# Kernel optimization log

Hardware: AMD Instinct MI355X
Metric: run time of the kernel (lower is better)

## Reference

```python
import jax, jax.numpy as jnp
import numpy as np

# ---- module constants (from init_kwargs) ----
L = 16            # num_levels
T = 524288        # table_size (power of 2 -> uint32 wraparound-safe mod)
DIN = 3
FPL = 2           # FEATURES_PER_LEVEL
GRID_MIN, GRID_MAX = -1.0, 1.0
B = 262144

RES = jnp.asarray(np.exp(np.linspace(np.log(16.0), np.log(2048.0), L)), dtype=jnp.float32)  # (L,)
PRIMES = jnp.array([1, 2654435761, 805459861], dtype=jnp.uint32)                            # (3,)
# offsets match torch: format(i, '03b') -> MSB first
OFFSETS = jnp.array([[(i >> (DIN - 1 - d)) & 1 for d in range(DIN)] for i in range(2 ** DIN)], dtype=jnp.uint32)  # (8,3)
OFF_F = OFFSETS.astype(jnp.float32)
OFF_HASH = (OFFSETS * PRIMES).sum(-1)  # (8,) uint32; hash is linear in coords so corner offsets separate out


def setup_inputs() -> dict:
    key = jax.random.key(0)
    ks = jax.random.split(key, 8)
    return {
        "x": jax.random.uniform(ks[0], (B, DIN), jnp.float32, minval=GRID_MIN, maxval=GRID_MAX),
        "embeddings": jax.random.uniform(ks[1], (L, T, FPL), jnp.float32, minval=-1e-4, maxval=1e-4),
        "W1": jax.random.normal(ks[2], (64, L * FPL), jnp.float32) * (1.0 / np.sqrt(L * FPL)),
        "b1": jax.random.normal(ks[3], (64,), jnp.float32) * 0.01,
        "W2": jax.random.normal(ks[4], (64, 64), jnp.float32) * (1.0 / 8.0),
        "b2": jax.random.normal(ks[5], (64,), jnp.float32) * 0.01,
        "Wout": jax.random.normal(ks[6], (1, 64), jnp.float32) * (1.0 / 8.0),
        "bout": jax.random.normal(ks[7], (1,), jnp.float32) * 0.01,
    }


def reference(x, embeddings, W1, b1, W2, b2, Wout, bout):
    n = x.shape[0]
    x_norm = (x - GRID_MIN) / (GRID_MAX - GRID_MIN)          # (B,3) in [0,1)
    x_grid = x_norm[None, :, :] * RES[:, None, None]          # (L,B,3)
    x0 = jnp.floor(x_grid)
    w = x_grid - x0                                           # (L,B,3) fractional part
    # hashed = ((x0+offset) . primes) % T ; linear -> split base + offset hash (uint32 wrap == low bits of int64)
    base = (x0.astype(jnp.uint32) * PRIMES).sum(-1)           # (L,B)
    hashed = ((base[:, :, None] + OFF_HASH) % T).astype(jnp.int32)   # (L,B,8)
    corners = jnp.take_along_axis(
        embeddings, hashed.reshape(L, -1, 1), axis=1
    ).reshape(L, n, 2 ** DIN, FPL)                            # (L,B,8,2)
    # trilinear weights: prod over dims of (1-off) + w*(2*off-1)
    per_dim = 1.0 - OFF_F + w[:, :, None, :] * (2.0 * OFF_F - 1.0)   # (L,B,8,3)
    cw = per_dim.prod(-1)                                     # (L,B,8)
    value = jnp.einsum('lbc,lbcf->lbf', cw, corners)          # (L,B,2)
    encoded = jnp.moveaxis(value, 0, 1).reshape(n, L * FPL)   # (B,32)
    h = jax.nn.silu(encoded @ W1.T + b1)
    h = jax.nn.silu(h @ W2.T + b2)
    return (h @ Wout.T + bout).squeeze(-1)                    # (B,)
```

## Files before the change

kernel.cpp:

```cpp
#include <hip/hip_runtime.h>
#include <math.h>
#include <stdint.h>

#define NLEV 16
#define TBL 524288
#define TMASK (TBL - 1)
#define BLOCK 256
#define SPT 4
#define P1 2654435761u
#define P2 805459861u

struct ResArr { float r[NLEV]; };

typedef __attribute__((ext_vector_type(4))) float f32x4;
typedef __attribute__((ext_vector_type(8))) short bf16x8;
struct __attribute__((packed, aligned(8))) f4wrap { f32x4 v; };

__device__ __forceinline__ float silu_f(float v) {
    return __fdividef(v, 1.0f + __expf(-v));
}

__device__ __forceinline__ uint32_t f2bf(float f) {
    uint32_t u = __float_as_uint(f);
    return (u + 0x7FFFu + ((u >> 16) & 1u)) >> 16;
}
__device__ __forceinline__ float bf2f(uint32_t b) {
    return __uint_as_float(b << 16);
}
__device__ __forceinline__ void split_bf(float x, bf16x8& hi, bf16x8& lo, int e) {
    const uint32_t hb = f2bf(x);
    hi[e] = (short)hb;
    lo[e] = (short)f2bf(x - bf2f(hb));
}

__global__ void __launch_bounds__(BLOCK)
encode_kernel(const float* __restrict__ x,
              const float* __restrict__ emb,
              uint32_t* __restrict__ enc_ws,
              int nsamp, ResArr res)
{
    const int bid = blockIdx.x;
    const int xcd = bid & 7;
    const int j   = bid >> 3;
    int lvl, chunk;
    if (j < 352) {
        const int F = xcd * 352 + j;
        lvl = 5 + (F >> 8);
        chunk = F & 255;
    } else {
        const int C = xcd * 160 + (j - 352);
        lvl = C >> 8;
        chunk = C & 255;
    }

    const int t  = threadIdx.x;
    const int s0 = chunk * (BLOCK * SPT) + t;
    const float rs = res.r[lvl];
    const float* tabf = emb + (size_t)lvl * TBL * 2;

    uint32_t i0[SPT][4];
    float w0[SPT], w1[SPT], w2[SPT];
    uint32_t bad = 0;

    #pragma unroll
    for (int p = 0; p < SPT; ++p) {
        const int s = s0 + p * BLOCK;
        const float xv0 = __builtin_nontemporal_load(&x[(size_t)s * 3 + 0]);
        const float xv1 = __builtin_nontemporal_load(&x[(size_t)s * 3 + 1]);
        const float xv2 = __builtin_nontemporal_load(&x[(size_t)s * 3 + 2]);
        const float g0 = (xv0 + 1.0f) * 0.5f * rs;
        const float g1 = (xv1 + 1.0f) * 0.5f * rs;
        const float g2 = (xv2 + 1.0f) * 0.5f * rs;
        const float f0 = floorf(g0), f1 = floorf(g1), f2 = floorf(g2);
        w0[p] = g0 - f0; w1[p] = g1 - f1; w2[p] = g2 - f2;
        const uint32_t hb = (uint32_t)f0 + (uint32_t)f1 * P1 + (uint32_t)f2 * P2;
        #pragma unroll
        for (int q = 0; q < 4; ++q) {
            uint32_t h = hb;
            if ((q >> 1) & 1) h += P1;
            if (q & 1)        h += P2;
            i0[p][q] = h & TMASK;
            bad |= (uint32_t)(i0[p][q] == TMASK);
        }
    }

    f32x4 v[SPT][4];
    if (__builtin_expect(__any((int)bad), 0)) {
        #pragma unroll
        for (int p = 0; p < SPT; ++p)
            #pragma unroll
            for (int q = 0; q < 4; ++q) {
                const uint32_t a = i0[p][q];
                const uint32_t b = (a + 1u) & TMASK;
                const float2 lo = *(const float2*)(tabf + 2 * (size_t)a);
                const float2 hi = *(const float2*)(tabf + 2 * (size_t)b);
                v[p][q] = f32x4{lo.x, lo.y, hi.x, hi.y};
            }
    } else {
        #pragma unroll
        for (int p = 0; p < SPT; ++p)
            #pragma unroll
            for (int q = 0; q < 4; ++q)
                v[p][q] = ((const f4wrap*)(tabf + 2 * (size_t)i0[p][q]))->v;
    }

    #pragma unroll
    for (int p = 0; p < SPT; ++p) {
        const float om0 = 1.0f - w0[p], om1 = 1.0f - w1[p], om2 = 1.0f - w2[p];
        float e0 = 0.0f, e1 = 0.0f;
        #pragma unroll
        for (int q = 0; q < 4; ++q) {
            float wb = (((q >> 1) & 1) ? w1[p] : om1) * ((q & 1) ? w2[p] : om2);
            const float c0 = om0 * wb;
            const float c1 = w0[p] * wb;
            e0 = fmaf(c0, v[p][q].x, fmaf(c1, v[p][q].z, e0));
            e1 = fmaf(c0, v[p][q].y, fmaf(c1, v[p][q].w, e1));
        }
        const int s = s0 + p * BLOCK;
        const uint32_t pk = f2bf(e0) | (f2bf(e1) << 16);
        __builtin_nontemporal_store(pk, &enc_ws[(size_t)lvl * nsamp + s]);
    }
}

__global__ void __launch_bounds__(BLOCK)
mlp_mfma_kernel(const uint32_t* __restrict__ enc_ws,
                const float* __restrict__ W1,
                const float* __restrict__ b1,
                const float* __restrict__ W2,
                const float* __restrict__ b2,
                const float* __restrict__ Wout,
                const float* __restrict__ bout,
                float* __restrict__ out, int nsamp)
{
    __shared__ __align__(16) unsigned short hbuf[4][32 * 72];

    const int tid  = threadIdx.x;
    const int wid  = tid >> 6;
    const int lane = tid & 63;
    const int l15  = lane & 15;
    const int g    = lane >> 4;
    const int sbase = blockIdx.x * 128 + wid * 32;
    unsigned short* hw = hbuf[wid];

    bf16x8 b1hi[4], b1lo[4];
    float  b1v[4];
    #pragma unroll
    for (int n = 0; n < 4; ++n) {
        const float* wr = W1 + (n * 16 + l15) * 32 + g * 8;
        const f32x4 wv0 = ((const f4wrap*)wr)->v;
        const f32x4 wv1 = ((const f4wrap*)(wr + 4))->v;
        #pragma unroll
        for (int e = 0; e < 4; ++e) {
            split_bf(wv0[e], b1hi[n], b1lo[n], e);
            split_bf(wv1[e], b1hi[n], b1lo[n], e + 4);
        }
        b1v[n] = b1[n * 16 + l15];
    }

    #pragma unroll
    for (int m = 0; m < 2; ++m) {
        union { uint32_t u[4]; bf16x8 v; } af;
        const int s = sbase + m * 16 + l15;
        #pragma unroll
        for (int d = 0; d < 4; ++d)
            af.u[d] = enc_ws[(size_t)(g * 4 + d) * nsamp + s];
        #pragma unroll
        for (int n = 0; n < 4; ++n) {
            f32x4 acc = {0.f, 0.f, 0.f, 0.f};
            acc = __builtin_amdgcn_mfma_f32_16x16x32_bf16(af.v, b1lo[n], acc, 0, 0, 0);
            acc = __builtin_amdgcn_mfma_f32_16x16x32_bf16(af.v, b1hi[n], acc, 0, 0, 0);
            #pragma unroll
            for (int r = 0; r < 4; ++r) {
                const int row = m * 16 + g * 4 + r;
                const int col = n * 16 + l15;
                hw[row * 72 + col] = (unsigned short)f2bf(silu_f(acc[r] + b1v[n]));
            }
        }
    }

    f32x4 acc2[2][4];
    #pragma unroll
    for (int m = 0; m < 2; ++m)
        #pragma unroll
        for (int n = 0; n < 4; ++n)
            acc2[m][n] = f32x4{0.f, 0.f, 0.f, 0.f};

    #pragma unroll
    for (int ks = 0; ks < 2; ++ks) {
        bf16x8 b2hi[4], b2lo[4];
        #pragma unroll
        for (int n = 0; n < 4; ++n) {
            const float* wr = W2 + (n * 16 + l15) * 64 + ks * 32 + g * 8;
            const f32x4 wv0 = ((const f4wrap*)wr)->v;
            const f32x4 wv1 = ((const f4wrap*)(wr + 4))->v;
            #pragma unroll
            for (int e = 0; e < 4; ++e) {
                split_bf(wv0[e], b2hi[n], b2lo[n], e);
                split_bf(wv1[e], b2hi[n], b2lo[n], e + 4);
            }
        }
        #pragma unroll
        for (int m = 0; m < 2; ++m) {
            const bf16x8 a2 = *(const bf16x8*)&hw[(m * 16 + l15) * 72 + ks * 32 + g * 8];
            #pragma unroll
            for (int n = 0; n < 4; ++n) {
                acc2[m][n] = __builtin_amdgcn_mfma_f32_16x16x32_bf16(a2, b2lo[n], acc2[m][n], 0, 0, 0);
                acc2[m][n] = __builtin_amdgcn_mfma_f32_16x16x32_bf16(a2, b2hi[n], acc2[m][n], 0, 0, 0);
            }
        }
    }

    float b2v[4], wov[4];
    #pragma unroll
    for (int n = 0; n < 4; ++n) {
        b2v[n] = b2[n * 16 + l15];
        wov[n] = Wout[n * 16 + l15];
    }
    const float bo = bout[0];

    #pragma unroll
    for (int m = 0; m < 2; ++m) {
        float part[4] = {0.f, 0.f, 0.f, 0.f};
        #pragma unroll
        for (int n = 0; n < 4; ++n)
            #pragma unroll
            for (int r = 0; r < 4; ++r)
                part[r] += silu_f(acc2[m][n][r] + b2v[n]) * wov[n];
        #pragma unroll
        for (int mask = 1; mask <= 8; mask <<= 1)
            #pragma unroll
            for (int r = 0; r < 4; ++r)
                part[r] += __shfl_xor(part[r], mask, 64);
        if (l15 == 0) {
            #pragma unroll
            for (int r = 0; r < 4; ++r)
                out[sbase + m * 16 + g * 4 + r] = part[r] + bo;
        }
    }
}

__global__ void __launch_bounds__(BLOCK)
hashgrid_mlp_kernel(const float* __restrict__ x,
                    const float* __restrict__ emb,
                    const float* __restrict__ W1,
                    const float* __restrict__ b1,
                    const float* __restrict__ W2,
                    const float* __restrict__ b2,
                    const float* __restrict__ Wout,
                    const float* __restrict__ bout,
                    float* __restrict__ out,
                    ResArr res)
{
    const int t = threadIdx.x;
    const int s = blockIdx.x * BLOCK + t;

    const float xn0 = (x[(size_t)s * 3 + 0] + 1.0f) * 0.5f;
    const float xn1 = (x[(size_t)s * 3 + 1] + 1.0f) * 0.5f;
    const float xn2 = (x[(size_t)s * 3 + 2] + 1.0f) * 0.5f;

    float enc[2 * NLEV];
    #pragma unroll
    for (int l = 0; l < NLEV; ++l) {
        const float rs = res.r[l];
        const float g0 = xn0 * rs, g1 = xn1 * rs, g2 = xn2 * rs;
        const float f0 = floorf(g0), f1 = floorf(g1), f2 = floorf(g2);
        const float w0 = g0 - f0, w1 = g1 - f1, w2 = g2 - f2;
        const uint32_t hb = (uint32_t)f0 + (uint32_t)f1 * P1 + (uint32_t)f2 * P2;
        const float2* tab = (const float2*)emb + (size_t)l * TBL;
        const float om0 = 1.0f - w0, om1 = 1.0f - w1, om2 = 1.0f - w2;
        float e0 = 0.0f, e1 = 0.0f;
        #pragma unroll
        for (int c = 0; c < 8; ++c) {
            const uint32_t cb0 = (c >> 2) & 1, cb1 = (c >> 1) & 1, cb2 = c & 1;
            uint32_t h = hb;
            if (cb0) h += 1u;
            if (cb1) h += P1;
            if (cb2) h += P2;
            h &= TMASK;
            const float2 vv = tab[h];
            float wt = (cb0 ? w0 : om0) * (cb1 ? w1 : om1);
            wt *= (cb2 ? w2 : om2);
            e0 = fmaf(wt, vv.x, e0);
            e1 = fmaf(wt, vv.y, e1);
        }
        enc[2 * l + 0] = e0;
        enc[2 * l + 1] = e1;
    }

    float h1[64];
    #pragma unroll
    for (int i = 0; i < 64; ++i) {
        float acc = b1[i];
        #pragma unroll
        for (int k = 0; k < 32; ++k)
            acc = fmaf(enc[k], W1[i * 32 + k], acc);
        h1[i] = silu_f(acc);
    }
    float o = bout[0];
    #pragma unroll
    for (int i = 0; i < 64; ++i) {
        float acc = b2[i];
        #pragma unroll
        for (int k = 0; k < 64; ++k)
            acc = fmaf(h1[k], W2[i * 64 + k], acc);
        o = fmaf(silu_f(acc), Wout[i], o);
    }
    out[s] = o;
}

extern "C" void kernel_launch(void* const* d_in, const int* in_sizes, int n_in,
                              void* d_out, int out_size, void* d_ws, size_t ws_size,
                              hipStream_t stream) {
    const float* x    = (const float*)d_in[0];
    const float* emb  = (const float*)d_in[1];
    const float* W1   = (const float*)d_in[2];
    const float* b1   = (const float*)d_in[3];
    const float* W2   = (const float*)d_in[4];
    const float* b2   = (const float*)d_in[5];
    const float* Wout = (const float*)d_in[6];
    const float* bout = (const float*)d_in[7];
    float* out = (float*)d_out;

    ResArr res;
    const double lg0 = log(16.0), lg1 = log(2048.0);
    for (int i = 0; i < NLEV; ++i)
        res.r[i] = (float)exp(lg0 + (lg1 - lg0) * (double)i / 15.0);

    const int n = in_sizes[0] / 3;
    const size_t ws_needed = (size_t)n * NLEV * sizeof(uint32_t);

    if (ws_size >= ws_needed) {
        uint32_t* enc_ws = (uint32_t*)d_ws;
        dim3 gridA(4096);
        encode_kernel<<<gridA, BLOCK, 0, stream>>>(x, emb, enc_ws, n, res);
        dim3 gridB(n / 128);
        mlp_mfma_kernel<<<gridB, BLOCK, 0, stream>>>(enc_ws, W1, b1, W2, b2,
                                                     Wout, bout, out, n);
    } else {
        dim3 grid(n / BLOCK);
        hashgrid_mlp_kernel<<<grid, BLOCK, 0, stream>>>(x, emb, W1, b1, W2, b2,
                                                        Wout, bout, out, res);
    }
}
```

Measured before the change: 129.4 us.

## Split batch into quarters and overlap encode with MLP in fused launches

Splits the samples into four quarters and software-pipelines the work: each fused launch encodes quarter q while running the MFMA MLP on quarter q-1, with separate prologue and epilogue launches. The goal is to overlap the memory-bound hash gather with the compute-bound MLP so neither phase leaves the GPU idle. In exchange there are five launches instead of two, every fused block reserves MLP shared memory even when it only encodes, and the encode per-XCD level mapping is rescaled to 64 chunks per quarter.

```diff
diff --git a/kernel.cpp b/kernel.cpp
--- a/kernel.cpp
+++ b/kernel.cpp
@@ -10,6 +10,11 @@
 #define P1 2654435761u
 #define P2 805459861u
 
+#define NQ 4
+#define QSAMP 65536
+#define ENC_BLOCKS 1024
+#define MLP_BLOCKS 512
+
 struct ResArr { float r[NLEV]; };
 
 typedef __attribute__((ext_vector_type(4))) float f32x4;
@@ -33,26 +38,20 @@
     lo[e] = (short)f2bf(x - bf2f(hb));
 }
 
-__global__ void __launch_bounds__(BLOCK)
-encode_kernel(const float* __restrict__ x,
-              const float* __restrict__ emb,
-              uint32_t* __restrict__ enc_ws,
-              int nsamp, ResArr res)
-{
-    const int bid = blockIdx.x;
+__device__ __forceinline__ void enc_map(int bid, int q, int& lvl, int& chunk) {
     const int xcd = bid & 7;
     const int j   = bid >> 3;
-    int lvl, chunk;
-    if (j < 352) {
-        const int F = xcd * 352 + j;
-        lvl = 5 + (F >> 8);
-        chunk = F & 255;
-    } else {
-        const int C = xcd * 160 + (j - 352);
-        lvl = C >> 8;
-        chunk = C & 255;
-    }
-
+    if (j < 88) { const int F = xcd * 88 + j;        lvl = 5 + (F >> 6); chunk = F & 63; }
+    else        { const int C = xcd * 40 + (j - 88); lvl = C >> 6;       chunk = C & 63; }
+    chunk += q * 64;
+}
+
+__device__ __forceinline__ void encode_body(const float* __restrict__ x,
+                                            const float* __restrict__ emb,
+                                            uint32_t* __restrict__ enc_ws,
+                                            int nsamp, const ResArr& res,
+                                            int lvl, int chunk)
+{
     const int t  = threadIdx.x;
     const int s0 = chunk * (BLOCK * SPT) + t;
     const float rs = res.r[lvl];
@@ -122,25 +121,23 @@
     }
 }
 
-__global__ void __launch_bounds__(BLOCK)
-mlp_mfma_kernel(const uint32_t* __restrict__ enc_ws,
-                const float* __restrict__ W1,
-                const float* __restrict__ b1,
-                const float* __restrict__ W2,
-                const float* __restrict__ b2,
-                const float* __restrict__ Wout,
-                const float* __restrict__ bout,
-                float* __restrict__ out, int nsamp)
-{
-    __shared__ __align__(16) unsigned short hbuf[4][32 * 72];
-
+__device__ __forceinline__ void mlp_body(const uint32_t* __restrict__ enc_ws,
+                                         const float* __restrict__ W1,
+                                         const float* __restrict__ b1,
+                                         const float* __restrict__ W2,
+                                         const float* __restrict__ b2,
+                                         const float* __restrict__ Wout,
+                                         const float* __restrict__ bout,
+                                         float* __restrict__ out, int nsamp,
+                                         int sbase0, unsigned short* hbuf)
+{
     const int tid  = threadIdx.x;
     const int wid  = tid >> 6;
     const int lane = tid & 63;
     const int l15  = lane & 15;
     const int g    = lane >> 4;
-    const int sbase = blockIdx.x * 128 + wid * 32;
-    unsigned short* hw = hbuf[wid];
+    const int sbase = sbase0 + wid * 32;
+    unsigned short* hw = hbuf + wid * (32 * 72);
 
     bf16x8 b1hi[4], b1lo[4];
     float  b1v[4];
@@ -237,6 +234,47 @@
                 out[sbase + m * 16 + g * 4 + r] = part[r] + bo;
         }
     }
+}
+
+__global__ void __launch_bounds__(BLOCK)
+encode_q_kernel(const float* __restrict__ x, const float* __restrict__ emb,
+                uint32_t* __restrict__ enc_ws, int nsamp, ResArr res, int q)
+{
+    int lvl, chunk;
+    enc_map(blockIdx.x, q, lvl, chunk);
+    encode_body(x, emb, enc_ws, nsamp, res, lvl, chunk);
+}
+
+__global__ void __launch_bounds__(BLOCK)
+fused_q_kernel(const float* __restrict__ x, const float* __restrict__ emb,
+               uint32_t* __restrict__ enc_ws,
+               const float* __restrict__ W1, const float* __restrict__ b1,
+               const float* __restrict__ W2, const float* __restrict__ b2,
+               const float* __restrict__ Wout, const float* __restrict__ bout,
+               float* __restrict__ out, int nsamp, ResArr res, int qe, int qm)
+{
+    __shared__ __align__(16) unsigned short hbuf[4 * 32 * 72];
+    if (blockIdx.x < ENC_BLOCKS) {
+        int lvl, chunk;
+        enc_map(blockIdx.x, qe, lvl, chunk);
+        encode_body(x, emb, enc_ws, nsamp, res, lvl, chunk);
+    } else {
+        const int mbid = blockIdx.x - ENC_BLOCKS;
+        mlp_body(enc_ws, W1, b1, W2, b2, Wout, bout, out, nsamp,
+                 qm * QSAMP + mbid * 128, hbuf);
+    }
+}
+
+__global__ void __launch_bounds__(BLOCK)
+mlp_q_kernel(const uint32_t* __restrict__ enc_ws,
+             const float* __restrict__ W1, const float* __restrict__ b1,
+             const float* __restrict__ W2, const float* __restrict__ b2,
+             const float* __restrict__ Wout, const float* __restrict__ bout,
+             float* __restrict__ out, int nsamp, int q)
+{
+    __shared__ __align__(16) unsigned short hbuf[4 * 32 * 72];
+    mlp_body(enc_ws, W1, b1, W2, b2, Wout, bout, out, nsamp,
+             q * QSAMP + blockIdx.x * 128, hbuf);
 }
 
 __global__ void __launch_bounds__(BLOCK)
@@ -329,13 +367,14 @@
     const int n = in_sizes[0] / 3;
     const size_t ws_needed = (size_t)n * NLEV * sizeof(uint32_t);
 
-    if (ws_size >= ws_needed) {
+    if (ws_size >= ws_needed && n == NQ * QSAMP) {
         uint32_t* enc_ws = (uint32_t*)d_ws;
-        dim3 gridA(4096);
-        encode_kernel<<<gridA, BLOCK, 0, stream>>>(x, emb, enc_ws, n, res);
-        dim3 gridB(n / 128);
-        mlp_mfma_kernel<<<gridB, BLOCK, 0, stream>>>(enc_ws, W1, b1, W2, b2,
-                                                     Wout, bout, out, n);
+        encode_q_kernel<<<dim3(ENC_BLOCKS), BLOCK, 0, stream>>>(x, emb, enc_ws, n, res, 0);
+        for (int q = 1; q < NQ; ++q)
+            fused_q_kernel<<<dim3(ENC_BLOCKS + MLP_BLOCKS), BLOCK, 0, stream>>>(
+                x, emb, enc_ws, W1, b1, W2, b2, Wout, bout, out, n, res, q, q - 1);
+        mlp_q_kernel<<<dim3(MLP_BLOCKS), BLOCK, 0, stream>>>(
+            enc_ws, W1, b1, W2, b2, Wout, bout, out, n, NQ - 1);
     } else {
         dim3 grid(n / BLOCK);
         hashgrid_mlp_kernel<<<grid, BLOCK, 0, stream>>>(x, emb, W1, b1, W2, b2,
```

Result: slower. 160.6 us (+24.1%).
